# Optimization experiments

Measured on AMD Instinct MI355X. Metric: run time of the kernel, lower is better.

## Reference

```python
import jax, jax.numpy as jnp
import numpy as np

LN_EPS = 1e-12


def setup_inputs() -> dict:
    key = jax.random.key(0)
    ks = jax.random.split(key, 5)
    b, t, n, di, do, de = 2, 3, 4096, 64, 64, 64
    return {
        "x": jax.random.normal(ks[0], (b, t, n, di), dtype=jnp.float32),
        "node_emb": jax.random.normal(ks[1], (n, de), dtype=jnp.float32),
        "time_emb": jax.random.normal(ks[2], (b, t, de), dtype=jnp.float32),
        "weights_pool": jax.random.normal(ks[3], (de, 2, di, do), dtype=jnp.float32) * 0.05,
        "bias_pool": jax.random.normal(ks[4], (de, do), dtype=jnp.float32) * 0.05,
        "ln_gamma": jnp.ones((de,), dtype=jnp.float32),
        "ln_beta": jnp.zeros((de,), dtype=jnp.float32),
    }


def reference(x, node_emb, time_emb, weights_pool, bias_pool, ln_gamma, ln_beta):
    # x: (b,t,n,di); node_emb: (n,de); time_emb: (b,t,de)
    # Dropout is identity in eval mode.
    e = node_emb[None, None, :, :] + time_emb[:, :, None, :]          # (b,t,n,de)
    mu = jnp.mean(e, axis=-1, keepdims=True)
    var = jnp.var(e, axis=-1, keepdims=True)
    e = (e - mu) * jax.lax.rsqrt(var + LN_EPS) * ln_gamma + ln_beta    # LayerNorm
    # Dynamic adjacency: softmax over source nodes
    supports2 = jax.nn.softmax(jnp.einsum("btnd,btmd->btnm", e, e), axis=-1)
    # supports1 is the identity matrix -> x_g1 == x
    x_g1 = x
    x_g2 = jnp.einsum("btnm,btmc->btnc", supports2, x)
    x_g = jnp.stack([x_g1, x_g2], axis=3)                              # (b,t,n,k=2,di)
    # Hypernetwork weights: node embeddings are identical for every t,
    # so tnd,dkio->tnkio reduces to nd,dkio->nkio (broadcast over t).
    weights = jnp.einsum("nd,dkio->nkio", node_emb, weights_pool)      # (n,2,di,do)
    bias = jnp.einsum("btd,do->bto", time_emb, bias_pool)              # (b,t,do)
    out = jnp.einsum("btnki,nkio->btno", x_g, weights) + bias[:, :, None, :]
    return out
```

## Files before the change

kernel.cpp:

```cpp
#include <hip/hip_runtime.h>


using bf16x8 = __attribute__((ext_vector_type(8))) __bf16;
using f32x4  = __attribute__((ext_vector_type(4))) float;
using f32x16 = __attribute__((ext_vector_type(16))) float;
using u32x4  = __attribute__((ext_vector_type(4))) unsigned int;

__device__ __forceinline__ unsigned short f2bf_bits(float f) {
    unsigned int u = __float_as_uint(f);
    u += 0x7fffu + ((u >> 16) & 1u);
    return (unsigned short)(u >> 16);
}

__device__ __forceinline__ unsigned int PK(float a, float b) {
    return __builtin_amdgcn_perm(__float_as_uint(b), __float_as_uint(a),
                                 0x07060302u);
}

__device__ __forceinline__ f32x4 mfma16(bf16x8 a, bf16x8 b, f32x4 c) {
    return __builtin_amdgcn_mfma_f32_16x16x32_bf16(a, b, c, 0, 0, 0);
}
__device__ __forceinline__ f32x16 mfma32(bf16x8 a, bf16x8 b, f32x16 c) {
    return __builtin_amdgcn_mfma_f32_32x32x16_bf16(a, b, c, 0, 0, 0);
}
__device__ __forceinline__ f32x16 zero16() {
    f32x16 z;
    #pragma unroll
    for (int i = 0; i < 16; ++i) z[i] = 0.f;
    return z;
}

__global__ __launch_bounds__(256) void k_prep(const float* __restrict__ x,
                                              const float* __restrict__ node_emb,
                                              const float* __restrict__ time_emb,
                                              const float* __restrict__ wp,
                                              const float* __restrict__ bias_pool,
                                              const float* __restrict__ gamma,
                                              const float* __restrict__ beta,
                                              unsigned short* __restrict__ eT,
                                              unsigned short* __restrict__ vT,
                                              unsigned short* __restrict__ ne_bf,
                                              unsigned short* __restrict__ wpB,
                                              float* __restrict__ biasw) {
    __shared__ float tile[64 * 65];
    const int b = blockIdx.x;
    const int t = threadIdx.x;
    if (b < 1536) {
        int lane = t & 63;
        int row0 = b * 16 + ((t >> 6) << 2);
        float gm = gamma[lane], bb2 = beta[lane];
        #pragma unroll
        for (int ri = 0; ri < 4; ++ri) {
            int rowf = row0 + ri;
            int bt = rowf >> 12, row = rowf & 4095;
            float v = node_emb[(row << 6) | lane] + time_emb[(bt << 6) | lane];
            float s = v, s2 = v * v;
            #pragma unroll
            for (int off = 32; off; off >>= 1) {
                s  += __shfl_xor(s,  off);
                s2 += __shfl_xor(s2, off);
            }
            float mu  = s * 0.015625f;
            float var = s2 * 0.015625f - mu * mu;
            float r   = rsqrtf(var + 1e-12f);
            float o   = (v - mu) * r * gm + bb2;
            size_t idx = (size_t)bt * 262144 + ((row >> 5) << 11)
                       + ((lane >> 4) << 9) + (((lane >> 3) & 1) << 8)
                       + ((row & 31) << 3) + (lane & 7);
            eT[idx] = f2bf_bits(o);
        }
    } else if (b < 1920) {
        int bb = b - 1536;
        int bt = bb >> 6, n0 = (bb & 63) << 6;
        const float* xr = x + ((size_t)((bt << 12) | n0) << 6);
        #pragma unroll
        for (int it = 0; it < 16; ++it) {
            int i = (it << 2) + (t >> 6);
            int d = t & 63;
            tile[i * 65 + d] = xr[(i << 6) + d];
        }
        __syncthreads();
        unsigned short* dst = vT + (size_t)bt * 262144;
        #pragma unroll
        for (int it = 0; it < 16; ++it) {
            int d = (it << 2) + (t >> 6);
            int n = t & 63;
            dst[(((n0 + n) >> 3) << 9) + (d << 3) + (n & 7)]
                = f2bf_bits(tile[n * 65 + d]);
        }
    } else if (b < 2944) {
        int idx = (b - 1920) * 256 + t;
        ne_bf[idx] = f2bf_bits(node_emb[idx]);
    } else if (b < 3072) {
        int ki = b - 2944;
        #pragma unroll
        for (int it = 0; it < 16; ++it) {
            int d = (it << 2) + (t >> 6);
            int o = t & 63;
            tile[d * 65 + o] = wp[(d << 13) + (ki << 6) + o];
        }
        __syncthreads();
        unsigned short* dst = wpB + ((size_t)ki << 12);
        #pragma unroll
        for (int it = 0; it < 2; ++it) {
            int u    = (it << 8) + t;
            int ot   = u >> 7;
            int frag = (u >> 6) & 1;
            int pos  = u & 63;
            int quad = pos >> 4, l16 = pos & 15;
            unsigned short* dp = dst + ((((ot << 1) + frag) << 9) + (pos << 3));
            #pragma unroll
            for (int j = 0; j < 8; ++j)
                dp[j] = f2bf_bits(
                    tile[((frag << 5) + (quad << 3) + j) * 65 + (ot << 4) + l16]);
        }
    } else {
        for (int idx = t; idx < 384; idx += 256) {
            int bt = idx >> 6, o = idx & 63;
            float bsum = 0.f;
            for (int d = 0; d < 64; ++d)
                bsum += time_emb[(bt << 6) + d] * bias_pool[(d << 6) + o];
            biasw[idx] = bsum;
        }
    }
}

__global__ __launch_bounds__(256, 2) void k_attn(const unsigned short* __restrict__ eT,
                                                 const unsigned short* __restrict__ vT,
                                                 float* __restrict__ P0,
                                                 float* __restrict__ P1,
                                                 float* __restrict__ L0,
                                                 float* __restrict__ L1) {
    __shared__ __align__(16) float Obuf[2][64 * 68];
    __shared__ float l_s[4][64];
    const int tid  = threadIdx.x;
    const int w    = tid >> 6;
    const int lane = tid & 63;
    const int l32  = lane & 31;
    const int h    = lane >> 5;

    const int bid     = (int)blockIdx.x;
    const int logical = (bid & 7) * 96 + (bid >> 3);
    const int set     = logical >> 6;
    const int qc      = logical & 63;
    const int bt      = set >> 1;
    const int half    = set & 1;
    const int qbase   = qc << 6;

    const unsigned short* eb = eT + (size_t)bt * 262144;
    const unsigned short* vb = vT + (size_t)bt * 262144;
    float* Pout = half ? P1 : P0;
    float* Lout = half ? L1 : L0;

    const unsigned short* qp = eb + ((qbase >> 5) << 11) + (h << 8) + (l32 << 3);
    bf16x8 qf0[4], qf1[4];
    #pragma unroll
    for (int c = 0; c < 4; ++c) {
        bf16x8 q0 = *(const bf16x8*)(qp + (c << 9));
        bf16x8 q1 = *(const bf16x8*)(qp + 2048 + (c << 9));
        #pragma unroll
        for (int j = 0; j < 8; ++j) {
            q0[j] = (__bf16)((float)q0[j] * 1.44269504f);
            q1[j] = (__bf16)((float)q1[j] * 1.44269504f);
        }
        qf0[c] = q0;
        qf1[c] = q1;
    }

    f32x16 O00 = zero16(), O01 = zero16();
    f32x16 O10 = zero16(), O11 = zero16();
    float lsa0[4] = {0.f, 0.f, 0.f, 0.f};
    float lsa1[4] = {0.f, 0.f, 0.f, 0.f};

    const int kstart = (half << 11) + (w << 9);
    const unsigned short* krBase = eb + ((kstart >> 5) << 11) + (h << 8) + (l32 << 3);
    const unsigned short* vrBase = vb + ((kstart >> 3) << 9) + (h << 9) + (l32 << 3);

    bf16x8 kA0, kA1, kA2, kA3, vA0, vA1, vA2, vA3;
    bf16x8 kB0, kB1, kB2, kB3, vB0, vB1, vB2, vB3;

#define LOAD_GRP(gi, K0, K1, K2, K3, V0, V1, V2, V3)                    \
    {                                                                   \
        const unsigned short* kp = krBase + ((gi) << 11);               \
        const unsigned short* vp = vrBase + ((gi) << 11);               \
        K0 = *(const bf16x8*)(kp);                                      \
        K1 = *(const bf16x8*)(kp + 512);                                \
        K2 = *(const bf16x8*)(kp + 1024);                               \
        K3 = *(const bf16x8*)(kp + 1536);                               \
        V0 = *(const bf16x8*)(vp);                                      \
        V1 = *(const bf16x8*)(vp + 256);                                \
        V2 = *(const bf16x8*)(vp + 1024);                               \
        V3 = *(const bf16x8*)(vp + 1280);                               \
    }

#define QSET(QF, LSA, OA, OB, K0, K1, K2, K3, V0, V1, V2, V3)           \
    {                                                                   \
        f32x16 S = zero16();                                            \
        S = mfma32(K0, QF[0], S);                                       \
        S = mfma32(K1, QF[1], S);                                       \
        S = mfma32(K2, QF[2], S);                                       \
        S = mfma32(K3, QF[3], S);                                       \
        float p[16];                                                    \
        _Pragma("unroll")                                               \
        for (int r = 0; r < 16; ++r) p[r] = __builtin_amdgcn_exp2f(S[r]); \
        _Pragma("unroll")                                               \
        for (int r = 0; r < 4; ++r)                                     \
            LSA[r] += (p[r] + p[r + 4]) + (p[r + 8] + p[r + 12]);       \
        unsigned int Pa = PK(p[0], p[1]),   Pb = PK(p[2], p[3]);        \
        unsigned int Pc = PK(p[4], p[5]),   Pd = PK(p[6], p[7]);        \
        unsigned int Pe = PK(p[8], p[9]),   Pf = PK(p[10], p[11]);      \
        unsigned int Pg = PK(p[12], p[13]), Ph = PK(p[14], p[15]);      \
        unsigned int e0 = (unsigned int)__shfl_xor((int)(h ? Pa : Pc), 32); \
        unsigned int e1 = (unsigned int)__shfl_xor((int)(h ? Pb : Pd), 32); \
        unsigned int e2 = (unsigned int)__shfl_xor((int)(h ? Pe : Pg), 32); \
        unsigned int e3 = (unsigned int)__shfl_xor((int)(h ? Pf : Ph), 32); \
        u32x4 w0 = { h ? e0 : Pa, h ? e1 : Pb,                          \
                     h ? Pc : e0, h ? Pd : e1 };                        \
        u32x4 w1 = { h ? e2 : Pe, h ? e3 : Pf,                          \
                     h ? Pg : e2, h ? Ph : e3 };                        \
        bf16x8 pf0 = __builtin_bit_cast(bf16x8, w0);                    \
        bf16x8 pf1 = __builtin_bit_cast(bf16x8, w1);                    \
        OA = mfma32(pf0, V0, OA);                                       \
        OB = mfma32(pf0, V1, OB);                                       \
        OA = mfma32(pf1, V2, OA);                                       \
        OB = mfma32(pf1, V3, OB);                                       \
    }

#define COMPUTE_GRP(K0, K1, K2, K3, V0, V1, V2, V3)                     \
    QSET(qf0, lsa0, O00, O01, K0, K1, K2, K3, V0, V1, V2, V3)           \
    QSET(qf1, lsa1, O10, O11, K0, K1, K2, K3, V0, V1, V2, V3)

    LOAD_GRP(0, kA0, kA1, kA2, kA3, vA0, vA1, vA2, vA3);
    for (int gi = 0; gi < 14; gi += 2) {
        LOAD_GRP(gi + 1, kB0, kB1, kB2, kB3, vB0, vB1, vB2, vB3);
        COMPUTE_GRP(kA0, kA1, kA2, kA3, vA0, vA1, vA2, vA3);
        LOAD_GRP(gi + 2, kA0, kA1, kA2, kA3, vA0, vA1, vA2, vA3);
        COMPUTE_GRP(kB0, kB1, kB2, kB3, vB0, vB1, vB2, vB3);
    }
    LOAD_GRP(15, kB0, kB1, kB2, kB3, vB0, vB1, vB2, vB3);
    COMPUTE_GRP(kA0, kA1, kA2, kA3, vA0, vA1, vA2, vA3);
    COMPUTE_GRP(kB0, kB1, kB2, kB3, vB0, vB1, vB2, vB3);
#undef LOAD_GRP
#undef QSET
#undef COMPUTE_GRP

    float ls0 = (lsa0[0] + lsa0[1]) + (lsa0[2] + lsa0[3]);
    float ls1 = (lsa1[0] + lsa1[1]) + (lsa1[2] + lsa1[3]);
    float l2_0 = ls0 + __shfl_xor(ls0, 32);
    float l2_1 = ls1 + __shfl_xor(ls1, 32);
    if (h == 0) {
        l_s[w][l32]      = l2_0;
        l_s[w][l32 + 32] = l2_1;
    }
    float* buf = Obuf[w & 1];
    if (w < 2) {
        #pragma unroll
        for (int r = 0; r < 16; ++r) {
            int qrow = (r & 3) + ((r >> 2) << 3) + (h << 2);
            buf[qrow * 68 + l32]             = O00[r];
            buf[qrow * 68 + 32 + l32]        = O01[r];
            buf[(qrow + 32) * 68 + l32]      = O10[r];
            buf[(qrow + 32) * 68 + 32 + l32] = O11[r];
        }
    }
    __syncthreads();
    if (w >= 2) {
        #pragma unroll
        for (int r = 0; r < 16; ++r) {
            int qrow = (r & 3) + ((r >> 2) << 3) + (h << 2);
            buf[qrow * 68 + l32]             += O00[r];
            buf[qrow * 68 + 32 + l32]        += O01[r];
            buf[(qrow + 32) * 68 + l32]      += O10[r];
            buf[(qrow + 32) * 68 + 32 + l32] += O11[r];
        }
    }
    __syncthreads();
    {
        int q0 = tid >> 3;
        int d0 = (tid & 7) << 3;
        #pragma unroll
        for (int qh = 0; qh < 2; ++qh) {
            int q = q0 + (qh << 5);
            const float* b0 = Obuf[0] + q * 68 + d0;
            const float* b1 = Obuf[1] + q * 68 + d0;
            float* dst = Pout + (((size_t)(bt << 12) + qbase + q) << 6) + d0;
            #pragma unroll
            for (int i = 0; i < 8; ++i) dst[i] = b0[i] + b1[i];
            if ((tid & 7) == 0)
                Lout[(bt << 12) + qbase + q] =
                    l_s[0][q] + l_s[1][q] + l_s[2][q] + l_s[3][q];
        }
    }
}

__global__ __launch_bounds__(256, 2) void k_hyper(const float* __restrict__ x,
                                                  const float* __restrict__ P0,
                                                  const float* __restrict__ P1,
                                                  const float* __restrict__ L0,
                                                  const float* __restrict__ L1,
                                                  const unsigned short* __restrict__ ne_bf,
                                                  const unsigned short* __restrict__ wpB,
                                                  const float* __restrict__ bias_ws,
                                                  float* __restrict__ out) {
    __shared__ float smem[13056];
    __shared__ float invl_s[96];
    const int t    = threadIdx.x;
    const int w    = t >> 6;
    const int lane = t & 63;
    const int l16  = lane & 15;
    const int quad = lane >> 4;
    const int n0   = (blockIdx.x >> 1) << 4;
    const int oh   = blockIdx.x & 1;

    if (t < 96) {
        int bt = t % 6, nl = t / 6;
        int idx = (bt << 12) + n0 + nl;
        invl_s[t] = 1.f / (L0[idx] + L1[idx]);
    }
    __syncthreads();

    float* xg_s = smem + w * 3104;
    const int i0 = (w & 1) << 5;
    for (int it = 0; it < 48; ++it) {
        int j  = (it << 6) + lane;
        int kk = j & 31;
        int btnl = j >> 5;
        int bt = btnl % 6;
        int nl = btnl / 6;
        size_t idx = (((size_t)(bt << 12) + n0 + nl) << 6) + i0 + kk;
        float v;
        if (w < 2) v = x[idx];
        else       v = (P0[idx] + P1[idx]) * invl_s[btnl];
        xg_s[kk * 97 + btnl] = v;
    }
    __syncthreads();

    const unsigned short* nb = ne_bf + ((n0 + l16) << 6) + (quad << 3);
    bf16x8 a0 = *(const bf16x8*)(nb);
    bf16x8 a1 = *(const bf16x8*)(nb + 32);

    float oac[2][4][6];
    #pragma unroll
    for (int oc = 0; oc < 2; ++oc)
        #pragma unroll
        for (int r = 0; r < 4; ++r)
            #pragma unroll
            for (int bt = 0; bt < 6; ++bt) oac[oc][r][bt] = 0.f;

    const int ki_base = w << 5;
    #pragma unroll 2
    for (int kk = 0; kk < 32; ++kk) {
        const int ki = ki_base + kk;
        float g[4][6];
        #pragma unroll
        for (int r = 0; r < 4; ++r) {
            const float* gp = xg_s + kk * 97 + ((quad << 2) + r) * 6;
            #pragma unroll
            for (int bt = 0; bt < 6; ++bt) g[r][bt] = gp[bt];
        }
        #pragma unroll
        for (int oc = 0; oc < 2; ++oc) {
            const unsigned short* bp =
                wpB + ((((size_t)ki << 2) + (oh * 2 + oc)) << 10) + (lane << 3);
            bf16x8 b0 = *(const bf16x8*)(bp);
            bf16x8 b1 = *(const bf16x8*)(bp + 512);
            f32x4 wf = mfma16(a0, b0, f32x4{0.f, 0.f, 0.f, 0.f});
            wf = mfma16(a1, b1, wf);
            #pragma unroll
            for (int r = 0; r < 4; ++r)
                #pragma unroll
                for (int bt = 0; bt < 6; ++bt)
                    oac[oc][r][bt] += wf[r] * g[r][bt];
        }
    }

    __syncthreads();
    #pragma unroll
    for (int oc = 0; oc < 2; ++oc)
        #pragma unroll
        for (int r = 0; r < 4; ++r)
            #pragma unroll
            for (int bt = 0; bt < 6; ++bt)
                smem[w * 3264 + ((quad << 2) + r) * 204 + bt * 34 + (oc << 4) + l16]
                    = oac[oc][r][bt];
    __syncthreads();
    #pragma unroll
    for (int rr = 0; rr < 4; ++rr) {
        int nl = (w << 2) + rr;
        #pragma unroll
        for (int bp2 = 0; bp2 < 3; ++bp2) {
            int bt = bp2 * 2 + (lane >> 5);
            int ol = lane & 31;
            int o  = (oh << 5) + ol;
            int a  = nl * 204 + bt * 34 + ol;
            float v = smem[a] + smem[a + 3264] + smem[a + 6528] + smem[a + 9792]
                    + bias_ws[(bt << 6) + o];
            out[(((size_t)(bt << 12) + n0 + nl) << 6) + o] = v;
        }
    }
}

extern "C" void kernel_launch(void* const* d_in, const int* in_sizes, int n_in,
                              void* d_out, int out_size, void* d_ws, size_t ws_size,
                              hipStream_t stream) {
    const float* x         = (const float*)d_in[0];
    const float* node_emb  = (const float*)d_in[1];
    const float* time_emb  = (const float*)d_in[2];
    const float* wp        = (const float*)d_in[3];
    const float* bias_pool = (const float*)d_in[4];
    const float* gamma     = (const float*)d_in[5];
    const float* beta      = (const float*)d_in[6];
    float* out = (float*)d_out;

    char* wsb = (char*)d_ws;
    unsigned short* eT    = (unsigned short*)(wsb);
    unsigned short* vT    = (unsigned short*)(wsb + 3145728);
    float*          P0    = (float*)         (wsb + 6291456);
    float*          P1    = (float*)         (wsb + 12582912);
    unsigned short* wpB   = (unsigned short*)(wsb + 18874368);
    unsigned short* ne_bf = (unsigned short*)(wsb + 19922944);
    float*          biasw = (float*)         (wsb + 20447232);
    float*          L0    = (float*)         (wsb + 20448768);
    float*          L1    = (float*)         (wsb + 20547072);

    k_prep<<<3073, 256, 0, stream>>>(x, node_emb, time_emb, wp, bias_pool,
                                     gamma, beta, eT, vT, ne_bf, wpB, biasw);
    k_attn<<<768, 256, 0, stream>>>(eT, vT, P0, P1, L0, L1);
    k_hyper<<<512, 256, 0, stream>>>(x, P0, P1, L0, L1, ne_bf, wpB, biasw, out);
}
```

Measured before the change: 139.8 us.

## Process 32 nodes per k_hyper block to reuse weight-pool loads

The hypernetwork kernel now handles two 16-node groups per block instead of one. Each bf16 weight-pool fragment loaded from global memory feeds two MFMA chains, which halves weight traffic per node. To fit this, shared-memory buffers, the staging loop and the output reduction are doubled, and the grid shrinks from 512 to 256 blocks with launch bounds relaxed to one block per CU. The trade-off is less parallelism and latency hiding (256 blocks on the device) and higher register and LDS use per block.

```diff
diff --git a/kernel.cpp b/kernel.cpp
--- a/kernel.cpp
+++ b/kernel.cpp
@@ -293,7 +293,7 @@
     }
 }
 
-__global__ __launch_bounds__(256, 2) void k_hyper(const float* __restrict__ x,
+__global__ __launch_bounds__(256, 1) void k_hyper(const float* __restrict__ x,
                                                   const float* __restrict__ P0,
                                                   const float* __restrict__ P1,
                                                   const float* __restrict__ L0,
@@ -302,26 +302,27 @@
                                                   const unsigned short* __restrict__ wpB,
                                                   const float* __restrict__ bias_ws,
                                                   float* __restrict__ out) {
-    __shared__ float smem[13056];
-    __shared__ float invl_s[96];
+    __shared__ float smem[26112];
+    __shared__ float invl_s[192];
     const int t    = threadIdx.x;
     const int w    = t >> 6;
     const int lane = t & 63;
     const int l16  = lane & 15;
     const int quad = lane >> 4;
-    const int n0   = (blockIdx.x >> 1) << 4;
+    const int n0   = (blockIdx.x >> 1) << 5;
     const int oh   = blockIdx.x & 1;
 
-    if (t < 96) {
+    if (t < 192) {
         int bt = t % 6, nl = t / 6;
         int idx = (bt << 12) + n0 + nl;
         invl_s[t] = 1.f / (L0[idx] + L1[idx]);
     }
     __syncthreads();
 
-    float* xg_s = smem + w * 3104;
+    float* xg_s = smem + w * 6176;
     const int i0 = (w & 1) << 5;
-    for (int it = 0; it < 48; ++it) {
+    #pragma unroll 4
+    for (int it = 0; it < 96; ++it) {
         int j  = (it << 6) + lane;
         int kk = j & 31;
         int btnl = j >> 5;
@@ -331,32 +332,41 @@
         float v;
         if (w < 2) v = x[idx];
         else       v = (P0[idx] + P1[idx]) * invl_s[btnl];
-        xg_s[kk * 97 + btnl] = v;
+        xg_s[kk * 193 + btnl] = v;
     }
     __syncthreads();
 
     const unsigned short* nb = ne_bf + ((n0 + l16) << 6) + (quad << 3);
-    bf16x8 a0 = *(const bf16x8*)(nb);
-    bf16x8 a1 = *(const bf16x8*)(nb + 32);
-
-    float oac[2][4][6];
+    bf16x8 a00 = *(const bf16x8*)(nb);
+    bf16x8 a01 = *(const bf16x8*)(nb + 32);
+    const unsigned short* nb1 = nb + (16 << 6);
+    bf16x8 a10 = *(const bf16x8*)(nb1);
+    bf16x8 a11 = *(const bf16x8*)(nb1 + 32);
+
+    float oac[2][2][4][6];
     #pragma unroll
-    for (int oc = 0; oc < 2; ++oc)
-        #pragma unroll
-        for (int r = 0; r < 4; ++r)
-            #pragma unroll
-            for (int bt = 0; bt < 6; ++bt) oac[oc][r][bt] = 0.f;
+    for (int g = 0; g < 2; ++g)
+        #pragma unroll
+        for (int oc = 0; oc < 2; ++oc)
+            #pragma unroll
+            for (int r = 0; r < 4; ++r)
+                #pragma unroll
+                for (int bt = 0; bt < 6; ++bt) oac[g][oc][r][bt] = 0.f;
 
     const int ki_base = w << 5;
     #pragma unroll 2
     for (int kk = 0; kk < 32; ++kk) {
         const int ki = ki_base + kk;
-        float g[4][6];
+        float g0[4][6], g1[4][6];
         #pragma unroll
         for (int r = 0; r < 4; ++r) {
-            const float* gp = xg_s + kk * 97 + ((quad << 2) + r) * 6;
-            #pragma unroll
-            for (int bt = 0; bt < 6; ++bt) g[r][bt] = gp[bt];
+            const float* gp0 = xg_s + kk * 193 + ((quad << 2) + r) * 6;
+            const float* gp1 = gp0 + 96;
+            #pragma unroll
+            for (int bt = 0; bt < 6; ++bt) {
+                g0[r][bt] = gp0[bt];
+                g1[r][bt] = gp1[bt];
+            }
         }
         #pragma unroll
         for (int oc = 0; oc < 2; ++oc) {
@@ -364,36 +374,42 @@
                 wpB + ((((size_t)ki << 2) + (oh * 2 + oc)) << 10) + (lane << 3);
             bf16x8 b0 = *(const bf16x8*)(bp);
             bf16x8 b1 = *(const bf16x8*)(bp + 512);
-            f32x4 wf = mfma16(a0, b0, f32x4{0.f, 0.f, 0.f, 0.f});
-            wf = mfma16(a1, b1, wf);
+            f32x4 wf0 = mfma16(a00, b0, f32x4{0.f, 0.f, 0.f, 0.f});
+            wf0 = mfma16(a01, b1, wf0);
+            f32x4 wf1 = mfma16(a10, b0, f32x4{0.f, 0.f, 0.f, 0.f});
+            wf1 = mfma16(a11, b1, wf1);
+            #pragma unroll
+            for (int r = 0; r < 4; ++r)
+                #pragma unroll
+                for (int bt = 0; bt < 6; ++bt) {
+                    oac[0][oc][r][bt] += wf0[r] * g0[r][bt];
+                    oac[1][oc][r][bt] += wf1[r] * g1[r][bt];
+                }
+        }
+    }
+
+    __syncthreads();
+    #pragma unroll
+    for (int g = 0; g < 2; ++g)
+        #pragma unroll
+        for (int oc = 0; oc < 2; ++oc)
             #pragma unroll
             for (int r = 0; r < 4; ++r)
                 #pragma unroll
                 for (int bt = 0; bt < 6; ++bt)
-                    oac[oc][r][bt] += wf[r] * g[r][bt];
-        }
-    }
-
+                    smem[w * 6528 + ((g << 4) + (quad << 2) + r) * 204
+                         + bt * 34 + (oc << 4) + l16] = oac[g][oc][r][bt];
     __syncthreads();
     #pragma unroll
-    for (int oc = 0; oc < 2; ++oc)
-        #pragma unroll
-        for (int r = 0; r < 4; ++r)
-            #pragma unroll
-            for (int bt = 0; bt < 6; ++bt)
-                smem[w * 3264 + ((quad << 2) + r) * 204 + bt * 34 + (oc << 4) + l16]
-                    = oac[oc][r][bt];
-    __syncthreads();
-    #pragma unroll
-    for (int rr = 0; rr < 4; ++rr) {
-        int nl = (w << 2) + rr;
+    for (int rr = 0; rr < 8; ++rr) {
+        int nl = (w << 3) + rr;
         #pragma unroll
         for (int bp2 = 0; bp2 < 3; ++bp2) {
             int bt = bp2 * 2 + (lane >> 5);
             int ol = lane & 31;
             int o  = (oh << 5) + ol;
             int a  = nl * 204 + bt * 34 + ol;
-            float v = smem[a] + smem[a + 3264] + smem[a + 6528] + smem[a + 9792]
+            float v = smem[a] + smem[a + 6528] + smem[a + 13056] + smem[a + 19584]
                     + bias_ws[(bt << 6) + o];
             out[(((size_t)(bt << 12) + n0 + nl) << 6) + o] = v;
         }
@@ -426,5 +442,5 @@
     k_prep<<<3073, 256, 0, stream>>>(x, node_emb, time_emb, wp, bias_pool,
                                      gamma, beta, eT, vT, ne_bf, wpB, biasw);
     k_attn<<<768, 256, 0, stream>>>(eT, vT, P0, P1, L0, L1);
-    k_hyper<<<512, 256, 0, stream>>>(x, P0, P1, L0, L1, ne_bf, wpB, biasw, out);
-}
+    k_hyper<<<256, 256, 0, stream>>>(x, P0, P1, L0, L1, ne_bf, wpB, biasw, out);
+}
```

After: 156.6 us. 12.1% more time.

## Split k_hyper reduction across eight waves with vectorized staging loads

Applied to the files above, without the earlier changes.

Grows k_hyper from 4 to 8 waves per block, so each wave now covers 16 of the 128 input-channel rows instead of 32. The staging loop switches to float4 loads of x and the P0/P1 partial outputs. The cross-wave reduction becomes a store by the first four waves followed by LDS atomicAdds from the other four, which keeps shared-memory use unchanged. The goal is more latency hiding and shorter per-wave loops, at the cost of extra barriers, LDS atomics and tighter register limits from launch_bounds(512,4).

```diff
diff --git a/kernel.cpp b/kernel.cpp
--- a/kernel.cpp
+++ b/kernel.cpp
@@ -293,7 +293,7 @@
     }
 }
 
-__global__ __launch_bounds__(256, 2) void k_hyper(const float* __restrict__ x,
+__global__ __launch_bounds__(512, 4) void k_hyper(const float* __restrict__ x,
                                                   const float* __restrict__ P0,
                                                   const float* __restrict__ P1,
                                                   const float* __restrict__ L0,
@@ -302,14 +302,14 @@
                                                   const unsigned short* __restrict__ wpB,
                                                   const float* __restrict__ bias_ws,
                                                   float* __restrict__ out) {
-    __shared__ float smem[13056];
-    __shared__ float invl_s[96];
+    __shared__ float smem[13152];
+    float* invl_s = smem + 13056;
     const int t    = threadIdx.x;
     const int w    = t >> 6;
     const int lane = t & 63;
     const int l16  = lane & 15;
     const int quad = lane >> 4;
-    const int n0   = (blockIdx.x >> 1) << 4;
+    const int n0   = ((int)blockIdx.x >> 1) << 4;
     const int oh   = blockIdx.x & 1;
 
     if (t < 96) {
@@ -319,19 +319,29 @@
     }
     __syncthreads();
 
-    float* xg_s = smem + w * 3104;
-    const int i0 = (w & 1) << 5;
-    for (int it = 0; it < 48; ++it) {
-        int j  = (it << 6) + lane;
-        int kk = j & 31;
-        int btnl = j >> 5;
+    float* xg_s = smem + w * 1552;
+    const int i0  = (w & 3) << 4;
+    const int isP = w >> 2;
+    #pragma unroll
+    for (int it = 0; it < 6; ++it) {
+        int u    = (it << 6) + lane;
+        int btnl = u >> 2;
+        int c4   = (u & 3) << 2;
         int bt = btnl % 6;
         int nl = btnl / 6;
-        size_t idx = (((size_t)(bt << 12) + n0 + nl) << 6) + i0 + kk;
-        float v;
-        if (w < 2) v = x[idx];
-        else       v = (P0[idx] + P1[idx]) * invl_s[btnl];
-        xg_s[kk * 97 + btnl] = v;
+        size_t idx = (((size_t)(bt << 12) + n0 + nl) << 6) + i0 + c4;
+        f32x4 v;
+        if (!isP) {
+            v = *(const f32x4*)(x + idx);
+        } else {
+            f32x4 p0 = *(const f32x4*)(P0 + idx);
+            f32x4 p1 = *(const f32x4*)(P1 + idx);
+            float il = invl_s[btnl];
+            #pragma unroll
+            for (int m = 0; m < 4; ++m) v[m] = (p0[m] + p1[m]) * il;
+        }
+        #pragma unroll
+        for (int m = 0; m < 4; ++m) xg_s[(c4 + m) * 97 + btnl] = v[m];
     }
     __syncthreads();
 
@@ -347,9 +357,9 @@
             #pragma unroll
             for (int bt = 0; bt < 6; ++bt) oac[oc][r][bt] = 0.f;
 
-    const int ki_base = w << 5;
-    #pragma unroll 2
-    for (int kk = 0; kk < 32; ++kk) {
+    const int ki_base = w << 4;
+    #pragma unroll 4
+    for (int kk = 0; kk < 16; ++kk) {
         const int ki = ki_base + kk;
         float g[4][6];
         #pragma unroll
@@ -375,18 +385,33 @@
     }
 
     __syncthreads();
+    if (w < 4) {
+        float* rp = smem + w * 3264;
+        #pragma unroll
+        for (int oc = 0; oc < 2; ++oc)
+            #pragma unroll
+            for (int r = 0; r < 4; ++r)
+                #pragma unroll
+                for (int bt = 0; bt < 6; ++bt)
+                    rp[((quad << 2) + r) * 204 + bt * 34 + (oc << 4) + l16]
+                        = oac[oc][r][bt];
+    }
+    __syncthreads();
+    if (w >= 4) {
+        float* rp = smem + (w & 3) * 3264;
+        #pragma unroll
+        for (int oc = 0; oc < 2; ++oc)
+            #pragma unroll
+            for (int r = 0; r < 4; ++r)
+                #pragma unroll
+                for (int bt = 0; bt < 6; ++bt)
+                    atomicAdd(&rp[((quad << 2) + r) * 204 + bt * 34
+                                  + (oc << 4) + l16], oac[oc][r][bt]);
+    }
+    __syncthreads();
     #pragma unroll
-    for (int oc = 0; oc < 2; ++oc)
-        #pragma unroll
-        for (int r = 0; r < 4; ++r)
-            #pragma unroll
-            for (int bt = 0; bt < 6; ++bt)
-                smem[w * 3264 + ((quad << 2) + r) * 204 + bt * 34 + (oc << 4) + l16]
-                    = oac[oc][r][bt];
-    __syncthreads();
-    #pragma unroll
-    for (int rr = 0; rr < 4; ++rr) {
-        int nl = (w << 2) + rr;
+    for (int rr = 0; rr < 2; ++rr) {
+        int nl = (w << 1) + rr;
         #pragma unroll
         for (int bp2 = 0; bp2 < 3; ++bp2) {
             int bt = bp2 * 2 + (lane >> 5);
@@ -426,5 +451,5 @@
     k_prep<<<3073, 256, 0, stream>>>(x, node_emb, time_emb, wp, bias_pool,
                                      gamma, beta, eT, vT, ne_bf, wpB, biasw);
     k_attn<<<768, 256, 0, stream>>>(eT, vT, P0, P1, L0, L1);
-    k_hyper<<<512, 256, 0, stream>>>(x, P0, P1, L0, L1, ne_bf, wpB, biasw, out);
-}
+    k_hyper<<<512, 512, 0, stream>>>(x, P0, P1, L0, L1, ne_bf, wpB, biasw, out);
+}
```

Measured after the change: 159.7 us. 1.14x slower.
